# Kernel optimization log

Measured on AMD Instinct MI355X. Metric: run time of the kernel, lower is better.

The kernel has to match this reference:

```python
import jax, jax.numpy as jnp
import numpy as np

D_MODEL = 512
D_STATE = 64
LN_EPS = 1e-3  # Keras LayerNormalization default epsilon


def setup_inputs() -> dict:
    key = jax.random.key(0)
    ks = jax.random.split(key, 12)
    B, S, D, N = 8, 4096, D_MODEL, D_STATE

    def glorot(k, shape):
        fan_in, fan_out = shape[0], shape[1]
        lim = np.sqrt(6.0 / (fan_in + fan_out)).astype(np.float32)
        return jax.random.uniform(k, shape, jnp.float32, -lim, lim)

    return {
        "x": jax.random.normal(ks[0], (B, S, D), jnp.float32),
        "ln_gamma": jnp.ones((D,), jnp.float32),
        "ln_beta": jnp.zeros((D,), jnp.float32),
        "W_in": glorot(ks[1], (D, D)),
        "b_in": jnp.zeros((D,), jnp.float32),
        "W_xs": glorot(ks[2], (D, N)),
        "W_B": glorot(ks[3], (D, N)),
        "b_B": jnp.zeros((N,), jnp.float32),
        "W_C": glorot(ks[4], (D, N)),
        "b_C": jnp.zeros((N,), jnp.float32),
        "A_log": jax.random.uniform(ks[5], (N,), jnp.float32, -4.0, -1.0),
        "D_skip": jnp.ones((D,), jnp.float32),
        "W_so": glorot(ks[6], (N, D)),
        "W_out": glorot(ks[7], (D, D)),
        "b_out": jnp.zeros((D,), jnp.float32),
    }


def reference(x, ln_gamma, ln_beta, W_in, b_in, W_xs, W_B, b_B, W_C, b_C,
              A_log, D_skip, W_so, W_out, b_out):
    residual = x
    # LayerNorm over last axis (Keras default eps=1e-3)
    mu = jnp.mean(x, axis=-1, keepdims=True)
    var = jnp.mean(jnp.square(x - mu), axis=-1, keepdims=True)
    xn = (x - mu) * jax.lax.rsqrt(var + LN_EPS) * ln_gamma + ln_beta
    # input projection (this projected x is what feeds the D skip too)
    xp = xn @ W_in + b_in                      # [B, S, D]
    Bmat = xp @ W_B + b_B                      # [B, S, N] selective B(x)
    Cmat = xp @ W_C + b_C                      # [B, S, N] selective C(x)
    xs = xp @ W_xs                             # [B, S, N]
    A_bar = jnp.exp(-jnp.exp(A_log))           # [N], stable decay in (0,1)
    Bx = Bmat * xs                             # per-step drive B_t * x_state_t

    # sequential scan: h_t = A_bar * h_{t-1} + Bx_t
    def step(h, bx):
        h = A_bar * h + bx
        return h, h

    h0 = jnp.zeros((x.shape[0], A_log.shape[0]), x.dtype)
    _, hs = jax.lax.scan(step, h0, jnp.swapaxes(Bx, 0, 1))  # hs: [S, B, N]
    hs = jnp.swapaxes(hs, 0, 1)                             # [B, S, N]

    y = jnp.einsum('bsn,nd->bsd', Cmat * hs, W_so) + D_skip * xp
    y = y @ W_out + b_out
    # dropout is identity at inference (training=None)
    return y + residual
```

## Files before the change

### kernel.cpp

```cpp
#include <hip/hip_runtime.h>
#include <cstdint>
#include <cstddef>


typedef unsigned short bf16_t;
typedef __attribute__((ext_vector_type(8))) short bh8;
typedef __attribute__((ext_vector_type(4))) float f4;

#define M_ROWS 32768
#define SCAN_L 32
#define SCAN_C 128

__device__ __forceinline__ unsigned short f2bf(float f) {
  union { float f; unsigned int u; } c; c.f = f;
  unsigned int u = c.u;
  return (unsigned short)((u + 0x7FFFu + ((u >> 16) & 1u)) >> 16);
}

__device__ __forceinline__ uint2 pack4bf(f4 a) {
  uint2 r;
  r.x = (unsigned)f2bf(a[0]) | ((unsigned)f2bf(a[1]) << 16);
  r.y = (unsigned)f2bf(a[2]) | ((unsigned)f2bf(a[3]) << 16);
  return r;
}

__device__ __forceinline__ void async_cp16(void* lds, const void* g) {
  __builtin_amdgcn_global_load_lds((const __attribute__((address_space(1))) void*)g,
                                   (__attribute__((address_space(3))) void*)lds, 16, 0, 0);
}

__global__ __launch_bounds__(256) void prep_all(
    const float* __restrict__ W_in, const float* __restrict__ W_out,
    const float* __restrict__ W_so, const float* __restrict__ W_xs,
    const float* __restrict__ W_B,  const float* __restrict__ W_C,
    const float* __restrict__ b_in, const float* __restrict__ D_skip,
    const float* __restrict__ A_log,
    bf16_t* __restrict__ Wout_t, bf16_t* __restrict__ Wdout_t,
    bf16_t* __restrict__ Win_b, bf16_t* __restrict__ Wso_b,
    bf16_t* __restrict__ Wcat_t, bf16_t* __restrict__ Wproj,
    float* __restrict__ Abar, float* __restrict__ Apow) {
  int i = blockIdx.x * 256 + threadIdx.x;
  if (i < 262144) { int k = i >> 9, n = i & 511;
    Wout_t[(size_t)n * 512 + k] = f2bf(W_out[k * 512 + n]); return; }
  i -= 262144;
  if (i < 262144) { int k = i >> 9, n = i & 511;
    Wdout_t[(size_t)n * 512 + k] = f2bf(D_skip[k] * W_out[k * 512 + n]); return; }
  i -= 262144;
  if (i < 262144) { Win_b[i] = f2bf(W_in[i]); return; }
  i -= 262144;
  if (i < 65536) { int r = i >> 9, j = i & 511;
    Win_b[(size_t)(512 + r) * 512 + j] = (r == 0) ? f2bf(b_in[j]) : (bf16_t)0; return; }
  i -= 65536;
  if (i < 65536) { int k = i >> 9, j = i & 511;
    Wso_b[i] = (k < 64) ? f2bf(W_so[k * 512 + j]) : (bf16_t)0; return; }
  i -= 65536;
  if (i < 131072) { int k = i >> 8, n = i & 255;
    float v = 0.f;
    if (n < 128) { int g = n >> 5, w = n & 31;
      v = (w < 16) ? W_xs[k * 64 + g * 16 + w] : W_B[k * 64 + g * 16 + (w - 16)];
    } else if (n < 192) v = W_C[k * 64 + n - 128];
    Wcat_t[(size_t)n * 512 + k] = f2bf(v); return; }
  i -= 131072;
  if (i < 32768) { int r = i >> 9, d = i & 511;
    Wproj[(size_t)(192 + r) * 512 + d] = 0; return; }
  i -= 32768;
  if (i < 64) {
    float a = __expf(A_log[i]);
    Abar[i] = __expf(-a);
    Apow[i] = __expf(-a * (float)SCAN_L);
  }
}

__global__ __launch_bounds__(256, 4) void gemm_prep(
    const bf16_t* __restrict__ Win_b, const bf16_t* __restrict__ Wcat_t,
    const bf16_t* __restrict__ Wso_b, const bf16_t* __restrict__ Wout_t,
    const bf16_t* __restrict__ Wdout_t,
    const float* __restrict__ b_B, const float* __restrict__ b_C,
    bf16_t* __restrict__ Wproj, bf16_t* __restrict__ Wcat2,
    float* __restrict__ biasp, float* __restrict__ biasW2) {
  __shared__ __align__(16) bf16_t As[128 * 64];
  __shared__ __align__(16) bf16_t Bs[128 * 64];
  const int tid = threadIdx.x;
  const int wave = tid >> 6, lane = tid & 63;
  const int quad = lane >> 4, l16 = lane & 15;
  const int wm = (wave >> 1) * 64, wn = (wave & 1) * 64;
  int role, mb, nb;
  if (blockIdx.x < 10)      { role = 0; mb = blockIdx.x >> 1; nb = blockIdx.x & 1; }
  else if (blockIdx.x < 14) { role = 1; mb = 0; nb = blockIdx.x - 10; }
  else { role = 2; int t = blockIdx.x - 14; mb = t >> 2; nb = t & 3; }
  const bf16_t* Ap = (role == 1) ? Wso_b : Win_b;
  const bf16_t* Bp = (role == 0) ? Wcat_t : (role == 1) ? Wout_t : Wdout_t;

  f4 acc[4][4];
  #pragma unroll
  for (int i = 0; i < 4; ++i)
    #pragma unroll
    for (int j = 0; j < 4; ++j) acc[i][j] = (f4){0.f, 0.f, 0.f, 0.f};

  for (int kt = 0; kt < 8; ++kt) {
    const int k0 = kt << 6;
    __syncthreads();
    #pragma unroll
    for (int i = 0; i < 4; ++i) {
      const int base = (wave * 4 + i) * 64;
      const int cid = base + lane;
      const int row = cid >> 3;
      const int g = (cid & 7) ^ (row & 7);
      async_cp16((char*)As + base * 16,
                 Ap + (size_t)(mb * 128 + row) * 512 + k0 + g * 8);
    }
    #pragma unroll
    for (int i = 0; i < 4; ++i) {
      const int base = (wave * 4 + i) * 64;
      const int cid = base + lane;
      const int row = cid >> 3;
      const int g = (cid & 7) ^ (row & 7);
      async_cp16((char*)Bs + base * 16,
                 Bp + (size_t)(nb * 128 + row) * 512 + k0 + g * 8);
    }
    __syncthreads();
    #pragma unroll
    for (int ks = 0; ks < 2; ++ks) {
      const int gb = ks * 4 + quad;
      bh8 af[4], bfv[4];
      #pragma unroll
      for (int im = 0; im < 4; ++im) {
        const int row = wm + im * 16 + l16;
        af[im] = *(const bh8*)((const char*)As + row * 128 + ((gb ^ (row & 7)) * 16));
      }
      #pragma unroll
      for (int in_ = 0; in_ < 4; ++in_) {
        const int row = wn + in_ * 16 + l16;
        bfv[in_] = *(const bh8*)((const char*)Bs + row * 128 + ((gb ^ (row & 7)) * 16));
      }
      #pragma unroll
      for (int im = 0; im < 4; ++im)
        #pragma unroll
        for (int in_ = 0; in_ < 4; ++in_)
          acc[im][in_] = __builtin_amdgcn_mfma_f32_16x16x32_bf16(af[im], bfv[in_],
                                                                 acc[im][in_], 0, 0, 0);
    }
  }

  #pragma unroll
  for (int im = 0; im < 4; ++im) {
    #pragma unroll
    for (int in_ = 0; in_ < 4; ++in_) {
      const int row0 = mb * 128 + wm + im * 16 + quad * 4;
      const int col = nb * 128 + wn + in_ * 16 + l16;
      if (role == 0) {
        if (col < 192) {
          if (row0 < 512) {
            *(uint2*)(Wproj + (size_t)col * 512 + row0) = pack4bf(acc[im][in_]);
          } else if (row0 == 512) {
            float v = acc[im][in_][0];
            if (col < 128) { int w = col & 31;
              if (w >= 16) v += b_B[(col >> 5) * 16 + (w - 16)];
            } else v += b_C[col - 128];
            biasp[col] = v;
          }
        }
      } else if (role == 1) {
        if (row0 < 64)
          *(uint2*)(Wcat2 + (size_t)col * 576 + row0) = pack4bf(acc[im][in_]);
      } else {
        if (row0 < 512) {
          *(uint2*)(Wcat2 + (size_t)col * 576 + 64 + row0) = pack4bf(acc[im][in_]);
        } else if (row0 == 512) {
          biasW2[col] = acc[im][in_][0];
        }
      }
    }
  }
}

__global__ __launch_bounds__(256) void ln_kernel(
    const float* __restrict__ x, const float* __restrict__ gamma,
    const float* __restrict__ beta, bf16_t* __restrict__ xn) {
  const int row = blockIdx.x * 4 + (threadIdx.x >> 6);
  const int lane = threadIdx.x & 63;
  const float* xr = x + (size_t)row * 512 + lane * 8;
  float4 v0 = *(const float4*)xr;
  float4 v1 = *(const float4*)(xr + 4);
  float s  = v0.x + v0.y + v0.z + v0.w + v1.x + v1.y + v1.z + v1.w;
  float sq = v0.x*v0.x + v0.y*v0.y + v0.z*v0.z + v0.w*v0.w
           + v1.x*v1.x + v1.y*v1.y + v1.z*v1.z + v1.w*v1.w;
  #pragma unroll
  for (int off = 32; off > 0; off >>= 1) {
    s  += __shfl_xor(s, off, 64);
    sq += __shfl_xor(sq, off, 64);
  }
  const float mu  = s * (1.0f / 512.0f);
  const float var = sq * (1.0f / 512.0f) - mu * mu;
  const float rs  = rsqrtf(var + 1e-3f);
  float4 g0 = *(const float4*)(gamma + lane * 8);
  float4 g1 = *(const float4*)(gamma + lane * 8 + 4);
  float4 b0 = *(const float4*)(beta + lane * 8);
  float4 b1 = *(const float4*)(beta + lane * 8 + 4);
  bh8 ov;
  ov[0] = (short)f2bf((v0.x - mu) * rs * g0.x + b0.x);
  ov[1] = (short)f2bf((v0.y - mu) * rs * g0.y + b0.y);
  ov[2] = (short)f2bf((v0.z - mu) * rs * g0.z + b0.z);
  ov[3] = (short)f2bf((v0.w - mu) * rs * g0.w + b0.w);
  ov[4] = (short)f2bf((v1.x - mu) * rs * g1.x + b1.x);
  ov[5] = (short)f2bf((v1.y - mu) * rs * g1.y + b1.y);
  ov[6] = (short)f2bf((v1.z - mu) * rs * g1.z + b1.z);
  ov[7] = (short)f2bf((v1.w - mu) * rs * g1.w + b1.w);
  *(bh8*)(xn + (size_t)row * 512 + lane * 8) = ov;
}

template <int MODE>
__global__ __launch_bounds__(256, 4) void gemm_mfma(
    const bf16_t* __restrict__ A0, const bf16_t* __restrict__ A1,
    const bf16_t* __restrict__ Wt, int K,
    float* __restrict__ outf,
    const float* __restrict__ bias0, const float* __restrict__ bias1,
    const float* __restrict__ resid) {
  __shared__ __align__(16) char smem[32768];
  bf16_t* As = (bf16_t*)smem;
  bf16_t* Bs = (bf16_t*)(smem + 16384);
  const int tid = threadIdx.x;
  const int wave = tid >> 6, lane = tid & 63;
  const int quad = lane >> 4, l16 = lane & 15;
  const int wm = (wave >> 1) * 64, wn = (wave & 1) * 64;
  const int mb = blockIdx.x, nb = blockIdx.y;

  f4 acc[4][4];
  #pragma unroll
  for (int i = 0; i < 4; ++i)
    #pragma unroll
    for (int j = 0; j < 4; ++j) acc[i][j] = (f4){0.f, 0.f, 0.f, 0.f};

  const int nkt = K >> 6;
  for (int kt = 0; kt < nkt; ++kt) {
    const int k0 = kt << 6;
    const bf16_t* Ap; int lda, kk;
    if (MODE == 3) {
      if (kt == 0) { Ap = A0; lda = 64;  kk = 0; }
      else         { Ap = A1; lda = 512; kk = k0 - 64; }
    } else { Ap = A0; lda = K; kk = k0; }

    __syncthreads();
    #pragma unroll
    for (int i = 0; i < 4; ++i) {
      const int base = (wave * 4 + i) * 64;
      const int cid = base + lane;
      const int row = cid >> 3;
      const int g = (cid & 7) ^ (row & 7);
      async_cp16((char*)As + base * 16,
                 Ap + (size_t)(mb * 128 + row) * lda + kk + g * 8);
    }
    #pragma unroll
    for (int i = 0; i < 4; ++i) {
      const int base = (wave * 4 + i) * 64;
      const int cid = base + lane;
      const int row = cid >> 3;
      const int g = (cid & 7) ^ (row & 7);
      async_cp16((char*)Bs + base * 16,
                 Wt + (size_t)(nb * 128 + row) * K + k0 + g * 8);
    }
    __syncthreads();

    #pragma unroll
    for (int ks = 0; ks < 2; ++ks) {
      const int gb = ks * 4 + quad;
      bh8 af[4], bfv[4];
      #pragma unroll
      for (int im = 0; im < 4; ++im) {
        const int row = wm + im * 16 + l16;
        af[im] = *(const bh8*)((const char*)As + row * 128 + ((gb ^ (row & 7)) * 16));
      }
      #pragma unroll
      for (int in_ = 0; in_ < 4; ++in_) {
        const int row = wn + in_ * 16 + l16;
        bfv[in_] = *(const bh8*)((const char*)Bs + row * 128 + ((gb ^ (row & 7)) * 16));
      }
      #pragma unroll
      for (int im = 0; im < 4; ++im)
        #pragma unroll
        for (int in_ = 0; in_ < 4; ++in_)
          acc[im][in_] = __builtin_amdgcn_mfma_f32_16x16x32_bf16(af[im], bfv[in_],
                                                                 acc[im][in_], 0, 0, 0);
    }
  }

  __syncthreads();
  float* lt = (float*)smem;

  if (MODE == 2) {
    if (nb == 0) {
      float* wb = lt + wave * 2048;
      #pragma unroll
      for (int im = 0; im < 4; ++im)
        #pragma unroll
        for (int pp = 0; pp < 2; ++pp)
          #pragma unroll
          for (int r = 0; r < 4; ++r) {
            const int c0 = wn + (2 * pp) * 16 + l16;
            const float vx = acc[im][2 * pp][r]     + bias1[c0];
            const float vb = acc[im][2 * pp + 1][r] + bias1[c0 + 16];
            wb[(im * 16 + quad * 4 + r) * 32 + pp * 16 + l16] = vx * vb;
          }
      const int rsub = lane >> 3, cg8 = lane & 7;
      #pragma unroll
      for (int rr = 0; rr < 8; ++rr) {
        const int rl = rr * 8 + rsub;
        f4 v = *(f4*)(wb + rl * 32 + cg8 * 4);
        const size_t row = (size_t)(mb * 128 + wm + rl);
        *(f4*)(outf + row * 64 + (wn >> 1) + cg8 * 4) = v;
      }
    } else if (wn == 0) {
      float* wb = lt + (wave >> 1) * 4096;
      #pragma unroll
      for (int im = 0; im < 4; ++im)
        #pragma unroll
        for (int in_ = 0; in_ < 4; ++in_)
          #pragma unroll
          for (int r = 0; r < 4; ++r) {
            const int c = in_ * 16 + l16;
            wb[(im * 16 + quad * 4 + r) * 64 + c] = acc[im][in_][r] + bias1[128 + c];
          }
      #pragma unroll
      for (int rr = 0; rr < 16; ++rr) {
        const int rl = rr * 4 + quad;
        f4 v = *(f4*)(wb + rl * 64 + l16 * 4);
        const size_t row = (size_t)(mb * 128 + wm + rl);
        *(f4*)(outf + ((size_t)M_ROWS + row) * 64 + l16 * 4) = v;
      }
    }
  } else {
    const int gcol = nb * 128 + wn + l16 * 4;
    f4 bsum = *(const f4*)(bias0 + gcol);
    bsum += *(const f4*)(bias1 + gcol);
    float* wb = lt + wave * 2048;
    #pragma unroll
    for (int p = 0; p < 2; ++p) {
      #pragma unroll
      for (int im2 = 0; im2 < 2; ++im2)
        #pragma unroll
        for (int in_ = 0; in_ < 4; ++in_)
          #pragma unroll
          for (int r = 0; r < 4; ++r)
            wb[(im2 * 16 + quad * 4 + r) * 64 + in_ * 16 + l16] = acc[p * 2 + im2][in_][r];
      #pragma unroll
      for (int rr = 0; rr < 8; ++rr) {
        const int rl = rr * 4 + quad;
        f4 v = *(f4*)(wb + rl * 64 + l16 * 4);
        const size_t row = (size_t)(mb * 128 + wm + p * 32 + rl);
        f4 rv = *(const f4*)(resid + row * 512 + gcol);
        f4 o = v + bsum + rv;
        __builtin_nontemporal_store(o, (f4*)(outf + row * 512 + gcol));
      }
    }
  }
}

__global__ __launch_bounds__(64) void scan_chunk(
    const float* __restrict__ projP, const float* __restrict__ Abar,
    float* __restrict__ carryT) {
  const int b = blockIdx.x >> 7, c = blockIdx.x & (SCAN_C - 1), n = threadIdx.x;
  const float A = Abar[n];
  const size_t row0 = (size_t)b * 4096 + c * SCAN_L;
  const float* pBx = projP + row0 * 64;
  float h = 0.f;
  for (int i = 0; i < SCAN_L; ++i)
    h = fmaf(A, h, pBx[i * 64 + n]);
  carryT[((size_t)(b * 64 + n)) * SCAN_C + c] = h;
}

__global__ __launch_bounds__(64) void scan_apply(
    const float* __restrict__ projP, const float* __restrict__ Abar,
    const float* __restrict__ Apow, const float* __restrict__ carryT,
    bf16_t* __restrict__ CH) {
  const int b = blockIdx.x >> 7, c = blockIdx.x & (SCAN_C - 1), n = threadIdx.x;
  const float A = Abar[n];
  const float Ap = Apow[n];
  const float* cr = carryT + ((size_t)(b * 64 + n)) * SCAN_C;
  float h = 0.f;
  for (int j = 0; j < c; ++j) h = fmaf(Ap, h, cr[j]);
  const size_t row0 = (size_t)b * 4096 + c * SCAN_L;
  const float* pBx = projP + row0 * 64;
  const float* pC  = projP + ((size_t)M_ROWS + row0) * 64;
  bf16_t* o = CH + row0 * 64;
  for (int i = 0; i < SCAN_L; ++i) {
    h = fmaf(A, h, pBx[i * 64 + n]);
    o[i * 64 + n] = f2bf(pC[i * 64 + n] * h);
  }
}

extern "C" void kernel_launch(void* const* d_in, const int* in_sizes, int n_in,
                              void* d_out, int out_size, void* d_ws, size_t ws_size,
                              hipStream_t stream) {
  const float* x      = (const float*)d_in[0];
  const float* ln_g   = (const float*)d_in[1];
  const float* ln_b   = (const float*)d_in[2];
  const float* W_in   = (const float*)d_in[3];
  const float* b_in   = (const float*)d_in[4];
  const float* W_xs   = (const float*)d_in[5];
  const float* W_B    = (const float*)d_in[6];
  const float* b_B    = (const float*)d_in[7];
  const float* W_C    = (const float*)d_in[8];
  const float* b_C    = (const float*)d_in[9];
  const float* A_log  = (const float*)d_in[10];
  const float* D_skip = (const float*)d_in[11];
  const float* W_so   = (const float*)d_in[12];
  const float* W_out  = (const float*)d_in[13];
  const float* b_out  = (const float*)d_in[14];
  float* out = (float*)d_out;

  char* w = (char*)d_ws;
  auto carve = [&](size_t bytes) {
    char* p = w; w += (bytes + 255) & ~(size_t)255; return p;
  };
  bf16_t* xn     = (bf16_t*)carve((size_t)M_ROWS * 512 * 2);
  float*  projP  = (float*)carve((size_t)2 * M_ROWS * 64 * 4);
  bf16_t* CH     = (bf16_t*)carve((size_t)M_ROWS * 64 * 2);
  float*  carryT = (float*)carve((size_t)8 * 64 * SCAN_C * 4);
  bf16_t* Wproj  = (bf16_t*)carve((size_t)256 * 512 * 2);
  bf16_t* Wcat2  = (bf16_t*)carve((size_t)512 * 576 * 2);
  bf16_t* Win_b  = (bf16_t*)carve((size_t)640 * 512 * 2);
  bf16_t* Wso_b  = (bf16_t*)carve((size_t)128 * 512 * 2);
  bf16_t* Wout_t = (bf16_t*)carve((size_t)512 * 512 * 2);
  bf16_t* Wdout_t= (bf16_t*)carve((size_t)512 * 512 * 2);
  bf16_t* Wcat_t = (bf16_t*)carve((size_t)256 * 512 * 2);
  float*  biasp  = (float*)carve(192 * 4);
  float*  biasW2 = (float*)carve(512 * 4);
  float*  Abar   = (float*)carve(256);
  float*  Apow   = (float*)carve(256);

  prep_all<<<4227, 256, 0, stream>>>(W_in, W_out, W_so, W_xs, W_B, W_C, b_in,
                                     D_skip, A_log, Wout_t, Wdout_t, Win_b,
                                     Wso_b, Wcat_t, Wproj, Abar, Apow);
  gemm_prep<<<34, 256, 0, stream>>>(Win_b, Wcat_t, Wso_b, Wout_t, Wdout_t,
                                    b_B, b_C, Wproj, Wcat2, biasp, biasW2);
  ln_kernel<<<8192, 256, 0, stream>>>(x, ln_g, ln_b, xn);
  gemm_mfma<2><<<dim3(256, 2), 256, 0, stream>>>(xn, nullptr, Wproj, 512,
                                                 projP, nullptr, biasp, nullptr);
  scan_chunk<<<8 * SCAN_C, 64, 0, stream>>>(projP, Abar, carryT);
  scan_apply<<<8 * SCAN_C, 64, 0, stream>>>(projP, Abar, Apow, carryT, CH);
  gemm_mfma<3><<<dim3(256, 4), 256, 0, stream>>>(CH, xn, Wcat2, 576,
                                                 out, b_out, biasW2, x);
}
```

Before: 240.5 us.

## Double-buffer GEMM A tiles, load B to registers, swizzle blocks per XCD, refine scan

The MFMA GEMM now double-buffers the A tile in LDS through async global-to-LDS copies. It loads the B operand straight from global memory into registers instead of staging it in LDS, and uses explicit vmcnt waits plus raw barriers so the next tile's copy overlaps the current tile's compute. Block indices are remapped so consecutive M tiles land on the same XCD, for better L2 locality. The scan uses 16-row chunks instead of 32, and its carry prefix loop is split into four independent FMA chains to add ILP. The cost is more global loads for B (each wave reads its own B fragments), hand-tuned waitcnt accounting that is fragile, and a lower occupancy hint.

```diff
diff --git a/kernel.cpp b/kernel.cpp
--- a/kernel.cpp
+++ b/kernel.cpp
@@ -8,8 +8,8 @@
 typedef __attribute__((ext_vector_type(4))) float f4;
 
 #define M_ROWS 32768
-#define SCAN_L 32
-#define SCAN_C 128
+#define SCAN_L 16
+#define SCAN_C 256
 
 __device__ __forceinline__ unsigned short f2bf(float f) {
   union { float f; unsigned int u; } c; c.f = f;
@@ -210,20 +210,23 @@
 }
 
 template <int MODE>
-__global__ __launch_bounds__(256, 4) void gemm_mfma(
+__global__ __launch_bounds__(256, 3) void gemm_mfma(
     const bf16_t* __restrict__ A0, const bf16_t* __restrict__ A1,
     const bf16_t* __restrict__ Wt, int K,
     float* __restrict__ outf,
     const float* __restrict__ bias0, const float* __restrict__ bias1,
     const float* __restrict__ resid) {
   __shared__ __align__(16) char smem[32768];
-  bf16_t* As = (bf16_t*)smem;
-  bf16_t* Bs = (bf16_t*)(smem + 16384);
   const int tid = threadIdx.x;
   const int wave = tid >> 6, lane = tid & 63;
   const int quad = lane >> 4, l16 = lane & 15;
   const int wm = (wave >> 1) * 64, wn = (wave & 1) * 64;
-  const int mb = blockIdx.x, nb = blockIdx.y;
+
+  const int bid = blockIdx.x;
+  const int xcd = bid & 7, t0 = bid >> 3;
+  int mb, nb;
+  if (MODE == 2) { nb = t0 & 1; mb = xcd * 32 + (t0 >> 1); }
+  else           { nb = t0 & 3; mb = xcd * 32 + (t0 >> 2); }
 
   f4 acc[4][4];
   #pragma unroll
@@ -232,56 +235,70 @@
     for (int j = 0; j < 4; ++j) acc[i][j] = (f4){0.f, 0.f, 0.f, 0.f};
 
   const int nkt = K >> 6;
-  for (int kt = 0; kt < nkt; ++kt) {
-    const int k0 = kt << 6;
+
+  auto stage = [&](int t, int b) {
     const bf16_t* Ap; int lda, kk;
     if (MODE == 3) {
-      if (kt == 0) { Ap = A0; lda = 64;  kk = 0; }
-      else         { Ap = A1; lda = 512; kk = k0 - 64; }
-    } else { Ap = A0; lda = K; kk = k0; }
-
-    __syncthreads();
+      if (t == 0) { Ap = A0; lda = 64;  kk = 0; }
+      else        { Ap = A1; lda = 512; kk = (t << 6) - 64; }
+    } else { Ap = A0; lda = 512; kk = t << 6; }
+    char* dst = (char*)smem + (b << 14);
     #pragma unroll
     for (int i = 0; i < 4; ++i) {
       const int base = (wave * 4 + i) * 64;
       const int cid = base + lane;
       const int row = cid >> 3;
       const int g = (cid & 7) ^ (row & 7);
-      async_cp16((char*)As + base * 16,
+      async_cp16(dst + base * 16,
                  Ap + (size_t)(mb * 128 + row) * lda + kk + g * 8);
     }
-    #pragma unroll
-    for (int i = 0; i < 4; ++i) {
-      const int base = (wave * 4 + i) * 64;
-      const int cid = base + lane;
-      const int row = cid >> 3;
-      const int g = (cid & 7) ^ (row & 7);
-      async_cp16((char*)Bs + base * 16,
-                 Wt + (size_t)(nb * 128 + row) * K + k0 + g * 8);
-    }
-    __syncthreads();
-
+  };
+
+  stage(0, 0);
+  asm volatile("" ::: "memory");
+
+  for (int kt = 0; kt < nkt; ++kt) {
+    const int cur = kt & 1;
+    const int k0 = kt << 6;
+
+    bh8 vB[2][4];
+    #pragma unroll
+    for (int ks = 0; ks < 2; ++ks)
+      #pragma unroll
+      for (int in_ = 0; in_ < 4; ++in_) {
+        const int row = wn + in_ * 16 + l16;
+        vB[ks][in_] = *(const bh8*)(Wt + (size_t)(nb * 128 + row) * K + k0 +
+                                    (ks * 4 + quad) * 8);
+      }
+
+    if (kt + 1 < nkt) {
+      stage(kt + 1, cur ^ 1);
+      asm volatile("s_waitcnt vmcnt(12)" ::: "memory");
+    } else {
+      asm volatile("s_waitcnt vmcnt(8)" ::: "memory");
+    }
+    __builtin_amdgcn_s_barrier();
+    if (kt + 1 < nkt) asm volatile("s_waitcnt vmcnt(4)" ::: "memory");
+    else              asm volatile("s_waitcnt vmcnt(0)" ::: "memory");
+
+    const char* bufp = (const char*)smem + (cur << 14);
     #pragma unroll
     for (int ks = 0; ks < 2; ++ks) {
       const int gb = ks * 4 + quad;
-      bh8 af[4], bfv[4];
+      bh8 af[4];
       #pragma unroll
       for (int im = 0; im < 4; ++im) {
         const int row = wm + im * 16 + l16;
-        af[im] = *(const bh8*)((const char*)As + row * 128 + ((gb ^ (row & 7)) * 16));
-      }
-      #pragma unroll
-      for (int in_ = 0; in_ < 4; ++in_) {
-        const int row = wn + in_ * 16 + l16;
-        bfv[in_] = *(const bh8*)((const char*)Bs + row * 128 + ((gb ^ (row & 7)) * 16));
+        af[im] = *(const bh8*)(bufp + row * 128 + ((gb ^ (row & 7)) * 16));
       }
       #pragma unroll
       for (int im = 0; im < 4; ++im)
         #pragma unroll
         for (int in_ = 0; in_ < 4; ++in_)
-          acc[im][in_] = __builtin_amdgcn_mfma_f32_16x16x32_bf16(af[im], bfv[in_],
+          acc[im][in_] = __builtin_amdgcn_mfma_f32_16x16x32_bf16(af[im], vB[ks][in_],
                                                                  acc[im][in_], 0, 0, 0);
     }
+    __builtin_amdgcn_s_barrier();
   }
 
   __syncthreads();
@@ -358,7 +375,7 @@
 __global__ __launch_bounds__(64) void scan_chunk(
     const float* __restrict__ projP, const float* __restrict__ Abar,
     float* __restrict__ carryT) {
-  const int b = blockIdx.x >> 7, c = blockIdx.x & (SCAN_C - 1), n = threadIdx.x;
+  const int b = blockIdx.x >> 8, c = blockIdx.x & (SCAN_C - 1), n = threadIdx.x;
   const float A = Abar[n];
   const size_t row0 = (size_t)b * 4096 + c * SCAN_L;
   const float* pBx = projP + row0 * 64;
@@ -372,12 +389,21 @@
     const float* __restrict__ projP, const float* __restrict__ Abar,
     const float* __restrict__ Apow, const float* __restrict__ carryT,
     bf16_t* __restrict__ CH) {
-  const int b = blockIdx.x >> 7, c = blockIdx.x & (SCAN_C - 1), n = threadIdx.x;
+  const int b = blockIdx.x >> 8, c = blockIdx.x & (SCAN_C - 1), n = threadIdx.x;
   const float A = Abar[n];
   const float Ap = Apow[n];
+  const float Ap4 = (Ap * Ap) * (Ap * Ap);
   const float* cr = carryT + ((size_t)(b * 64 + n)) * SCAN_C;
-  float h = 0.f;
-  for (int j = 0; j < c; ++j) h = fmaf(Ap, h, cr[j]);
+  float h0 = 0.f, h1 = 0.f, h2 = 0.f, h3 = 0.f;
+  int j = 0;
+  for (; j + 4 <= c; j += 4) {
+    h0 = fmaf(Ap4, h0, cr[j]);
+    h1 = fmaf(Ap4, h1, cr[j + 1]);
+    h2 = fmaf(Ap4, h2, cr[j + 2]);
+    h3 = fmaf(Ap4, h3, cr[j + 3]);
+  }
+  float h = fmaf(Ap, fmaf(Ap, fmaf(Ap, h0, h1), h2), h3);
+  for (; j < c; ++j) h = fmaf(Ap, h, cr[j]);
   const size_t row0 = (size_t)b * 4096 + c * SCAN_L;
   const float* pBx = projP + row0 * 64;
   const float* pC  = projP + ((size_t)M_ROWS + row0) * 64;
@@ -434,10 +460,10 @@
   gemm_prep<<<34, 256, 0, stream>>>(Win_b, Wcat_t, Wso_b, Wout_t, Wdout_t,
                                     b_B, b_C, Wproj, Wcat2, biasp, biasW2);
   ln_kernel<<<8192, 256, 0, stream>>>(x, ln_g, ln_b, xn);
-  gemm_mfma<2><<<dim3(256, 2), 256, 0, stream>>>(xn, nullptr, Wproj, 512,
-                                                 projP, nullptr, biasp, nullptr);
+  gemm_mfma<2><<<512, 256, 0, stream>>>(xn, nullptr, Wproj, 512,
+                                        projP, nullptr, biasp, nullptr);
   scan_chunk<<<8 * SCAN_C, 64, 0, stream>>>(projP, Abar, carryT);
   scan_apply<<<8 * SCAN_C, 64, 0, stream>>>(projP, Abar, Apow, carryT, CH);
-  gemm_mfma<3><<<dim3(256, 4), 256, 0, stream>>>(CH, xn, Wcat2, 576,
-                                                 out, b_out, biasW2, x);
-}
+  gemm_mfma<3><<<1024, 256, 0, stream>>>(CH, xn, Wcat2, 576,
+                                         out, b_out, biasW2, x);
+}
```

Result: slower. 255.7 us (+6.3%).

## Fuse chunk-scan carries into projection GEMM epilogue and merge LN with weight prep

Applied to the files above, without the earlier changes.

The per-chunk local scan (carry computation) now runs inside the projection GEMM epilogue on the Bx tile already held in LDS, which removes the separate scan_chunk kernel and its re-read of projP. Chunk length is halved to 16 and chunk count doubled. The carry prefix loop in scan_apply is split into four independent accumulators to break the serial dependency. LayerNorm is merged into the weight-prep GEMM launch to save a kernel launch, and the residual load becomes nontemporal. The cost is a longer serial carry prefix per chunk and a carry layout changed to be chunk-major.

```diff
diff --git a/kernel.cpp b/kernel.cpp
--- a/kernel.cpp
+++ b/kernel.cpp
@@ -8,8 +8,8 @@
 typedef __attribute__((ext_vector_type(4))) float f4;
 
 #define M_ROWS 32768
-#define SCAN_L 32
-#define SCAN_C 128
+#define SCAN_L 16
+#define SCAN_C 256
 
 __device__ __forceinline__ unsigned short f2bf(float f) {
   union { float f; unsigned int u; } c; c.f = f;
@@ -71,23 +71,61 @@
   }
 }
 
-__global__ __launch_bounds__(256, 4) void gemm_prep(
+__global__ __launch_bounds__(256, 4) void prep2_fused(
     const bf16_t* __restrict__ Win_b, const bf16_t* __restrict__ Wcat_t,
     const bf16_t* __restrict__ Wso_b, const bf16_t* __restrict__ Wout_t,
     const bf16_t* __restrict__ Wdout_t,
     const float* __restrict__ b_B, const float* __restrict__ b_C,
     bf16_t* __restrict__ Wproj, bf16_t* __restrict__ Wcat2,
-    float* __restrict__ biasp, float* __restrict__ biasW2) {
+    float* __restrict__ biasp, float* __restrict__ biasW2,
+    const float* __restrict__ x, const float* __restrict__ gamma,
+    const float* __restrict__ beta, bf16_t* __restrict__ xn) {
   __shared__ __align__(16) bf16_t As[128 * 64];
   __shared__ __align__(16) bf16_t Bs[128 * 64];
   const int tid = threadIdx.x;
+
+  if (blockIdx.x >= 34) {
+    const int row = (int)(blockIdx.x - 34) * 4 + (tid >> 6);
+    const int lane = tid & 63;
+    const float* xr = x + (size_t)row * 512 + lane * 8;
+    float4 v0 = *(const float4*)xr;
+    float4 v1 = *(const float4*)(xr + 4);
+    float s  = v0.x + v0.y + v0.z + v0.w + v1.x + v1.y + v1.z + v1.w;
+    float sq = v0.x*v0.x + v0.y*v0.y + v0.z*v0.z + v0.w*v0.w
+             + v1.x*v1.x + v1.y*v1.y + v1.z*v1.z + v1.w*v1.w;
+    #pragma unroll
+    for (int off = 32; off > 0; off >>= 1) {
+      s  += __shfl_xor(s, off, 64);
+      sq += __shfl_xor(sq, off, 64);
+    }
+    const float mu  = s * (1.0f / 512.0f);
+    const float var = sq * (1.0f / 512.0f) - mu * mu;
+    const float rs  = rsqrtf(var + 1e-3f);
+    float4 g0 = *(const float4*)(gamma + lane * 8);
+    float4 g1 = *(const float4*)(gamma + lane * 8 + 4);
+    float4 b0 = *(const float4*)(beta + lane * 8);
+    float4 b1 = *(const float4*)(beta + lane * 8 + 4);
+    bh8 ov;
+    ov[0] = (short)f2bf((v0.x - mu) * rs * g0.x + b0.x);
+    ov[1] = (short)f2bf((v0.y - mu) * rs * g0.y + b0.y);
+    ov[2] = (short)f2bf((v0.z - mu) * rs * g0.z + b0.z);
+    ov[3] = (short)f2bf((v0.w - mu) * rs * g0.w + b0.w);
+    ov[4] = (short)f2bf((v1.x - mu) * rs * g1.x + b1.x);
+    ov[5] = (short)f2bf((v1.y - mu) * rs * g1.y + b1.y);
+    ov[6] = (short)f2bf((v1.z - mu) * rs * g1.z + b1.z);
+    ov[7] = (short)f2bf((v1.w - mu) * rs * g1.w + b1.w);
+    *(bh8*)(xn + (size_t)row * 512 + lane * 8) = ov;
+    return;
+  }
+
+  const int bx = blockIdx.x;
   const int wave = tid >> 6, lane = tid & 63;
   const int quad = lane >> 4, l16 = lane & 15;
   const int wm = (wave >> 1) * 64, wn = (wave & 1) * 64;
   int role, mb, nb;
-  if (blockIdx.x < 10)      { role = 0; mb = blockIdx.x >> 1; nb = blockIdx.x & 1; }
-  else if (blockIdx.x < 14) { role = 1; mb = 0; nb = blockIdx.x - 10; }
-  else { role = 2; int t = blockIdx.x - 14; mb = t >> 2; nb = t & 3; }
+  if (bx < 10)      { role = 0; mb = bx >> 1; nb = bx & 1; }
+  else if (bx < 14) { role = 1; mb = 0; nb = bx - 10; }
+  else { role = 2; int t = bx - 14; mb = t >> 2; nb = t & 3; }
   const bf16_t* Ap = (role == 1) ? Wso_b : Win_b;
   const bf16_t* Bp = (role == 0) ? Wcat_t : (role == 1) ? Wout_t : Wdout_t;
 
@@ -174,48 +212,14 @@
   }
 }
 
-__global__ __launch_bounds__(256) void ln_kernel(
-    const float* __restrict__ x, const float* __restrict__ gamma,
-    const float* __restrict__ beta, bf16_t* __restrict__ xn) {
-  const int row = blockIdx.x * 4 + (threadIdx.x >> 6);
-  const int lane = threadIdx.x & 63;
-  const float* xr = x + (size_t)row * 512 + lane * 8;
-  float4 v0 = *(const float4*)xr;
-  float4 v1 = *(const float4*)(xr + 4);
-  float s  = v0.x + v0.y + v0.z + v0.w + v1.x + v1.y + v1.z + v1.w;
-  float sq = v0.x*v0.x + v0.y*v0.y + v0.z*v0.z + v0.w*v0.w
-           + v1.x*v1.x + v1.y*v1.y + v1.z*v1.z + v1.w*v1.w;
-  #pragma unroll
-  for (int off = 32; off > 0; off >>= 1) {
-    s  += __shfl_xor(s, off, 64);
-    sq += __shfl_xor(sq, off, 64);
-  }
-  const float mu  = s * (1.0f / 512.0f);
-  const float var = sq * (1.0f / 512.0f) - mu * mu;
-  const float rs  = rsqrtf(var + 1e-3f);
-  float4 g0 = *(const float4*)(gamma + lane * 8);
-  float4 g1 = *(const float4*)(gamma + lane * 8 + 4);
-  float4 b0 = *(const float4*)(beta + lane * 8);
-  float4 b1 = *(const float4*)(beta + lane * 8 + 4);
-  bh8 ov;
-  ov[0] = (short)f2bf((v0.x - mu) * rs * g0.x + b0.x);
-  ov[1] = (short)f2bf((v0.y - mu) * rs * g0.y + b0.y);
-  ov[2] = (short)f2bf((v0.z - mu) * rs * g0.z + b0.z);
-  ov[3] = (short)f2bf((v0.w - mu) * rs * g0.w + b0.w);
-  ov[4] = (short)f2bf((v1.x - mu) * rs * g1.x + b1.x);
-  ov[5] = (short)f2bf((v1.y - mu) * rs * g1.y + b1.y);
-  ov[6] = (short)f2bf((v1.z - mu) * rs * g1.z + b1.z);
-  ov[7] = (short)f2bf((v1.w - mu) * rs * g1.w + b1.w);
-  *(bh8*)(xn + (size_t)row * 512 + lane * 8) = ov;
-}
-
 template <int MODE>
 __global__ __launch_bounds__(256, 4) void gemm_mfma(
     const bf16_t* __restrict__ A0, const bf16_t* __restrict__ A1,
     const bf16_t* __restrict__ Wt, int K,
     float* __restrict__ outf,
     const float* __restrict__ bias0, const float* __restrict__ bias1,
-    const float* __restrict__ resid) {
+    const float* __restrict__ resid,
+    const float* __restrict__ Abar, float* __restrict__ carryT) {
   __shared__ __align__(16) char smem[32768];
   bf16_t* As = (bf16_t*)smem;
   bf16_t* Bs = (bf16_t*)(smem + 16384);
@@ -309,6 +313,22 @@
         const size_t row = (size_t)(mb * 128 + wm + rl);
         *(f4*)(outf + row * 64 + (wn >> 1) + cg8 * 4) = v;
       }
+      {
+        const int bb = mb >> 5;
+        const int cbase = (mb & 31) * 8 + (wm >> 4);
+        const int ch = lane & 31;
+        const int n = (wn >> 1) + ch;
+        const float A = Abar[n];
+        #pragma unroll
+        for (int t = 0; t < 2; ++t) {
+          const int cl = (lane >> 5) + 2 * t;
+          float hv = 0.f;
+          #pragma unroll
+          for (int i = 0; i < SCAN_L; ++i)
+            hv = fmaf(A, hv, wb[(cl * SCAN_L + i) * 32 + ch]);
+          carryT[(size_t)(cbase + cl) * 512 + bb * 64 + n] = hv;
+        }
+      }
     } else if (wn == 0) {
       float* wb = lt + (wave >> 1) * 4096;
       #pragma unroll
@@ -347,37 +367,33 @@
         const int rl = rr * 4 + quad;
         f4 v = *(f4*)(wb + rl * 64 + l16 * 4);
         const size_t row = (size_t)(mb * 128 + wm + p * 32 + rl);
-        f4 rv = *(const f4*)(resid + row * 512 + gcol);
+        f4 rv = __builtin_nontemporal_load((const f4*)(resid + row * 512 + gcol));
         f4 o = v + bsum + rv;
         __builtin_nontemporal_store(o, (f4*)(outf + row * 512 + gcol));
       }
     }
   }
-}
-
-__global__ __launch_bounds__(64) void scan_chunk(
-    const float* __restrict__ projP, const float* __restrict__ Abar,
-    float* __restrict__ carryT) {
-  const int b = blockIdx.x >> 7, c = blockIdx.x & (SCAN_C - 1), n = threadIdx.x;
-  const float A = Abar[n];
-  const size_t row0 = (size_t)b * 4096 + c * SCAN_L;
-  const float* pBx = projP + row0 * 64;
-  float h = 0.f;
-  for (int i = 0; i < SCAN_L; ++i)
-    h = fmaf(A, h, pBx[i * 64 + n]);
-  carryT[((size_t)(b * 64 + n)) * SCAN_C + c] = h;
 }
 
 __global__ __launch_bounds__(64) void scan_apply(
     const float* __restrict__ projP, const float* __restrict__ Abar,
     const float* __restrict__ Apow, const float* __restrict__ carryT,
     bf16_t* __restrict__ CH) {
-  const int b = blockIdx.x >> 7, c = blockIdx.x & (SCAN_C - 1), n = threadIdx.x;
+  const int b = blockIdx.x >> 8, c = blockIdx.x & (SCAN_C - 1), n = threadIdx.x;
   const float A = Abar[n];
   const float Ap = Apow[n];
-  const float* cr = carryT + ((size_t)(b * 64 + n)) * SCAN_C;
-  float h = 0.f;
-  for (int j = 0; j < c; ++j) h = fmaf(Ap, h, cr[j]);
+  const float Ap4 = (Ap * Ap) * (Ap * Ap);
+  const float* cr = carryT + b * 64 + n;
+  float h0 = 0.f, h1 = 0.f, h2 = 0.f, h3 = 0.f;
+  int j = 0;
+  for (; j + 4 <= c; j += 4) {
+    h0 = fmaf(Ap4, h0, cr[(size_t)j * 512]);
+    h1 = fmaf(Ap4, h1, cr[(size_t)(j + 1) * 512]);
+    h2 = fmaf(Ap4, h2, cr[(size_t)(j + 2) * 512]);
+    h3 = fmaf(Ap4, h3, cr[(size_t)(j + 3) * 512]);
+  }
+  float h = fmaf(Ap, fmaf(Ap, fmaf(Ap, h0, h1), h2), h3);
+  for (; j < c; ++j) h = fmaf(Ap, h, cr[(size_t)j * 512]);
   const size_t row0 = (size_t)b * 4096 + c * SCAN_L;
   const float* pBx = projP + row0 * 64;
   const float* pC  = projP + ((size_t)M_ROWS + row0) * 64;
@@ -415,7 +431,7 @@
   bf16_t* xn     = (bf16_t*)carve((size_t)M_ROWS * 512 * 2);
   float*  projP  = (float*)carve((size_t)2 * M_ROWS * 64 * 4);
   bf16_t* CH     = (bf16_t*)carve((size_t)M_ROWS * 64 * 2);
-  float*  carryT = (float*)carve((size_t)8 * 64 * SCAN_C * 4);
+  float*  carryT = (float*)carve((size_t)SCAN_C * 512 * 4);
   bf16_t* Wproj  = (bf16_t*)carve((size_t)256 * 512 * 2);
   bf16_t* Wcat2  = (bf16_t*)carve((size_t)512 * 576 * 2);
   bf16_t* Win_b  = (bf16_t*)carve((size_t)640 * 512 * 2);
@@ -431,13 +447,14 @@
   prep_all<<<4227, 256, 0, stream>>>(W_in, W_out, W_so, W_xs, W_B, W_C, b_in,
                                      D_skip, A_log, Wout_t, Wdout_t, Win_b,
                                      Wso_b, Wcat_t, Wproj, Abar, Apow);
-  gemm_prep<<<34, 256, 0, stream>>>(Win_b, Wcat_t, Wso_b, Wout_t, Wdout_t,
-                                    b_B, b_C, Wproj, Wcat2, biasp, biasW2);
-  ln_kernel<<<8192, 256, 0, stream>>>(x, ln_g, ln_b, xn);
+  prep2_fused<<<34 + 8192, 256, 0, stream>>>(Win_b, Wcat_t, Wso_b, Wout_t,
+                                             Wdout_t, b_B, b_C, Wproj, Wcat2,
+                                             biasp, biasW2, x, ln_g, ln_b, xn);
   gemm_mfma<2><<<dim3(256, 2), 256, 0, stream>>>(xn, nullptr, Wproj, 512,
-                                                 projP, nullptr, biasp, nullptr);
-  scan_chunk<<<8 * SCAN_C, 64, 0, stream>>>(projP, Abar, carryT);
+                                                 projP, nullptr, biasp, nullptr,
+                                                 Abar, carryT);
   scan_apply<<<8 * SCAN_C, 64, 0, stream>>>(projP, Abar, Apow, carryT, CH);
   gemm_mfma<3><<<dim3(256, 4), 256, 0, stream>>>(CH, xn, Wcat2, 576,
-                                                 out, b_out, biasW2, x);
-}
+                                                 out, b_out, biasW2, x,
+                                                 nullptr, nullptr);
+}
```

Result: faster. 222.7 us (-7.4%).
